# Kernel tuning notes

Measured on AMD Instinct MI355X. Metric: run time of the kernel, lower is better.

The kernel has to match this reference:

```python
import jax, jax.numpy as jnp
import numpy as np

B, D_OUT, SEQ = 4, 512, 4000
N_LABELS, E_DIM = 8929, 300


def setup_inputs() -> dict:
    key = jax.random.key(0)
    k1, k2, k3, k4 = jax.random.split(key, 4)
    H = jax.random.normal(k1, (B, D_OUT, SEQ), dtype=jnp.float32)
    label_emb = jax.random.normal(k2, (N_LABELS, E_DIM), dtype=jnp.float32)  # Q.weight
    W_map = jax.random.normal(k3, (D_OUT, E_DIM), dtype=jnp.float32) * 0.05  # conv1d k=1 weight [out,in]
    b_map = jax.random.normal(k4, (D_OUT,), dtype=jnp.float32) * 0.05
    return {"H": H, "label_emb": label_emb, "W_map": W_map, "b_map": b_map}


def reference(H, label_emb, W_map, b_map):
    # mapping_layer(Q.weight.T).T : kernel-size-1 conv == linear over embedding dim
    Q = jnp.einsum('oe,le->lo', W_map, label_emb) + b_map  # [n_labels, d_out]
    # E = Q @ H ; H is [b, d_out, seq] -> E [b, n_labels, seq] (scale=False)
    E = jnp.einsum('ld,bds->bls', Q, H)
    A = jax.nn.softmax(E, axis=2)                          # softmax over sequence
    C = jnp.einsum('bls,bds->bld', A, H)                   # A @ H^T -> [b, n_labels, d_out]
    return C, A
```

## Files before the change

kernel.cpp:

```cpp
#include <hip/hip_runtime.h>

#define BB 4
#define DD 512
#define SS 4000
#define LL 8929
#define EE 300

typedef __attribute__((ext_vector_type(8))) short bhalf8;
typedef __attribute__((ext_vector_type(4))) float floatx4;
typedef __attribute__((ext_vector_type(4))) unsigned short us4;

struct HS { unsigned short h, l; };

__device__ __forceinline__ HS splitR(float x) {
  unsigned u = __builtin_bit_cast(unsigned, x);
  unsigned hb = (u + 0x7FFFu + ((u >> 16) & 1u)) >> 16;
  float hf = __builtin_bit_cast(float, hb << 16);
  float r = x - hf;
  unsigned v = __builtin_bit_cast(unsigned, r);
  unsigned lb = (v + 0x7FFFu + ((v >> 16) & 1u)) >> 16;
  HS o; o.h = (unsigned short)hb; o.l = (unsigned short)lb;
  return o;
}

__device__ __forceinline__ HS splitT(float x) {
  unsigned u = __builtin_bit_cast(unsigned, x);
  float hf = __builtin_bit_cast(float, u & 0xFFFF0000u);
  float r = x - hf;
  HS o;
  o.h = (unsigned short)(u >> 16);
  o.l = (unsigned short)(__builtin_bit_cast(unsigned, r) >> 16);
  return o;
}

__device__ __forceinline__ void gld16(const unsigned short* g, void* l) {
  __builtin_amdgcn_global_load_lds(
      (const __attribute__((address_space(1))) unsigned int*)g,
      (__attribute__((address_space(3))) unsigned int*)l, 16, 0, 0);
}

__global__ __launch_bounds__(256) void gemm_e(
    const unsigned short* __restrict__ Qh, const unsigned short* __restrict__ Ql,
    const unsigned short* __restrict__ Hth, const unsigned short* __restrict__ Htl,
    float* __restrict__ Eg) {
  __shared__ __align__(16) unsigned short Ah_s[128 * 32];
  __shared__ __align__(16) unsigned short Al_s[128 * 32];
  __shared__ __align__(16) unsigned short Bh_s[128 * 32];
  __shared__ __align__(16) unsigned short Bl_s[128 * 32];

  const unsigned short* Bhp = Hth + (long)blockIdx.z * SS * DD;
  const unsigned short* Blp = Htl + (long)blockIdx.z * SS * DD;
  float* E = Eg + (long)blockIdx.z * LL * SS;

  const int t = threadIdx.x, lane = t & 63, w = t >> 6;
  const int m0 = blockIdx.y * 128, n0 = blockIdx.x * 128;
  const int wm = (w >> 1) * 64, wn = (w & 1) * 64;
  const int lr = lane & 15;

  const int srow = lane >> 2;
  const int sch = ((lane & 3) ^ ((lane >> 3) & 3)) * 8;
  const int r0 = w * 32 + srow, r1 = r0 + 16;
  const long am0 = (long)((m0 + r0 < LL) ? m0 + r0 : LL - 1) * DD;
  const long am1 = (long)((m0 + r1 < LL) ? m0 + r1 : LL - 1) * DD;
  const long bn0 = (long)((n0 + r0 < SS) ? n0 + r0 : SS - 1) * DD;
  const long bn1 = (long)((n0 + r1 < SS) ? n0 + r1 : SS - 1) * DD;
  char* const dA = (char*)Ah_s + w * 2048;
  char* const dAl = (char*)Al_s + w * 2048;
  char* const dB = (char*)Bh_s + w * 2048;
  char* const dBl = (char*)Bl_s + w * 2048;

  const int chA = (((lane >> 4) ^ ((lr >> 1) & 3))) * 16;
  const int raB = (wm + lr) * 64 + chA;
  const int rbB = (wn + lr) * 64 + chA;

  floatx4 acc[4][4];
#pragma unroll
  for (int i = 0; i < 4; ++i)
#pragma unroll
    for (int j = 0; j < 4; ++j) acc[i][j] = (floatx4){0.f, 0.f, 0.f, 0.f};

  for (int kb = 0; kb < DD; kb += 32) {
    __syncthreads();
    gld16(Qh + am0 + kb + sch, dA);
    gld16(Qh + am1 + kb + sch, dA + 1024);
    gld16(Ql + am0 + kb + sch, dAl);
    gld16(Ql + am1 + kb + sch, dAl + 1024);
    gld16(Bhp + bn0 + kb + sch, dB);
    gld16(Bhp + bn1 + kb + sch, dB + 1024);
    gld16(Blp + bn0 + kb + sch, dBl);
    gld16(Blp + bn1 + kb + sch, dBl + 1024);
    __syncthreads();

    bhalf8 ah[4], al[4], bh[4], bl[4];
#pragma unroll
    for (int f = 0; f < 4; ++f) {
      ah[f] = *(const bhalf8*)((const char*)Ah_s + raB + f * 1024);
      al[f] = *(const bhalf8*)((const char*)Al_s + raB + f * 1024);
      bh[f] = *(const bhalf8*)((const char*)Bh_s + rbB + f * 1024);
      bl[f] = *(const bhalf8*)((const char*)Bl_s + rbB + f * 1024);
    }
#pragma unroll
    for (int i = 0; i < 4; ++i)
#pragma unroll
      for (int j = 0; j < 4; ++j) {
        acc[i][j] = __builtin_amdgcn_mfma_f32_16x16x32_bf16(ah[i], bh[j], acc[i][j], 0, 0, 0);
        acc[i][j] = __builtin_amdgcn_mfma_f32_16x16x32_bf16(ah[i], bl[j], acc[i][j], 0, 0, 0);
        acc[i][j] = __builtin_amdgcn_mfma_f32_16x16x32_bf16(al[i], bh[j], acc[i][j], 0, 0, 0);
      }
  }

  const int cr = (lane >> 4) * 4;
#pragma unroll
  for (int i = 0; i < 4; ++i)
#pragma unroll
    for (int j = 0; j < 4; ++j)
#pragma unroll
      for (int r = 0; r < 4; ++r) {
        const int m = m0 + wm + i * 16 + cr + r;
        const int n = n0 + wn + j * 16 + lr;
        if (m < LL && n < SS) E[(long)m * SS + n] = acc[i][j][r];
      }
}

__global__ __launch_bounds__(256) void gemm_c(
    const float* __restrict__ Ag, const unsigned short* __restrict__ Hh,
    const unsigned short* __restrict__ Hl, float* __restrict__ Cg) {
  __shared__ __align__(16) unsigned short Ah_s[128][40];
  __shared__ __align__(16) unsigned short Al_s[128][40];
  __shared__ __align__(16) unsigned short Bh_s[128 * 32];
  __shared__ __align__(16) unsigned short Bl_s[128 * 32];

  const float* A = Ag + (long)blockIdx.z * LL * SS;
  const unsigned short* Bhp = Hh + (long)blockIdx.z * DD * SS;
  const unsigned short* Blp = Hl + (long)blockIdx.z * DD * SS;
  float* C = Cg + (long)blockIdx.z * LL * DD;

  const int t = threadIdx.x, lane = t & 63, w = t >> 6;
  const int m0 = blockIdx.y * 128, n0 = blockIdx.x * 128;
  const int wm = (w >> 1) * 64, wn = (w & 1) * 64;
  const int lr = lane & 15;

  const int srow = lane >> 2;
  const int sch = ((lane & 3) ^ ((lane >> 3) & 3)) * 8;
  const long bn0 = (long)(n0 + w * 32 + srow) * SS;
  const long bn1 = bn0 + (long)16 * SS;
  char* const dB = (char*)Bh_s + w * 2048;
  char* const dBl = (char*)Bl_s + w * 2048;

  const int sr = t >> 3;
  const int scol = (t & 7) * 4;

  const int chB = (((lane >> 4) ^ ((lr >> 1) & 3))) * 16;
  const int rbB = (wn + lr) * 64 + chB;
  const int raBytes = (lane >> 4) * 16;

  floatx4 acc[4][4];
#pragma unroll
  for (int i = 0; i < 4; ++i)
#pragma unroll
    for (int j = 0; j < 4; ++j) acc[i][j] = (floatx4){0.f, 0.f, 0.f, 0.f};

  for (int kb = 0; kb < SS; kb += 32) {
    __syncthreads();
    gld16(Bhp + bn0 + kb + sch, dB);
    gld16(Bhp + bn1 + kb + sch, dB + 1024);
    gld16(Blp + bn0 + kb + sch, dBl);
    gld16(Blp + bn1 + kb + sch, dBl + 1024);
#pragma unroll
    for (int rr = 0; rr < 4; ++rr) {
      const int row = rr * 32 + sr;
      const int m = m0 + row;
      float4 v = make_float4(0.f, 0.f, 0.f, 0.f);
      if (m < LL) v = *reinterpret_cast<const float4*>(A + (long)m * SS + kb + scol);
      HS p0 = splitT(v.x), p1 = splitT(v.y), p2 = splitT(v.z), p3 = splitT(v.w);
      us4 h, l;
      h.x = p0.h; l.x = p0.l; h.y = p1.h; l.y = p1.l;
      h.z = p2.h; l.z = p2.l; h.w = p3.h; l.w = p3.l;
      *reinterpret_cast<us4*>(&Ah_s[row][scol]) = h;
      *reinterpret_cast<us4*>(&Al_s[row][scol]) = l;
    }
    __syncthreads();

    bhalf8 ah[4], al[4], bh[4], bl[4];
#pragma unroll
    for (int f = 0; f < 4; ++f) {
      ah[f] = *(const bhalf8*)((const char*)&Ah_s[wm + f * 16 + lr][0] + raBytes);
      al[f] = *(const bhalf8*)((const char*)&Al_s[wm + f * 16 + lr][0] + raBytes);
      bh[f] = *(const bhalf8*)((const char*)Bh_s + rbB + f * 1024);
      bl[f] = *(const bhalf8*)((const char*)Bl_s + rbB + f * 1024);
    }
#pragma unroll
    for (int i = 0; i < 4; ++i)
#pragma unroll
      for (int j = 0; j < 4; ++j) {
        acc[i][j] = __builtin_amdgcn_mfma_f32_16x16x32_bf16(ah[i], bh[j], acc[i][j], 0, 0, 0);
        acc[i][j] = __builtin_amdgcn_mfma_f32_16x16x32_bf16(ah[i], bl[j], acc[i][j], 0, 0, 0);
        acc[i][j] = __builtin_amdgcn_mfma_f32_16x16x32_bf16(al[i], bh[j], acc[i][j], 0, 0, 0);
      }
  }

  const int cr = (lane >> 4) * 4;
#pragma unroll
  for (int i = 0; i < 4; ++i)
#pragma unroll
    for (int j = 0; j < 4; ++j)
#pragma unroll
      for (int r = 0; r < 4; ++r) {
        const int m = m0 + wm + i * 16 + cr + r;
        const int n = n0 + wn + j * 16 + lr;
        if (m < LL) C[(long)m * DD + n] = acc[i][j][r];
      }
}

__global__ __launch_bounds__(256) void split_transpose(
    const float* __restrict__ H, unsigned short* __restrict__ Th,
    unsigned short* __restrict__ Tl) {
  __shared__ float tile[32][33];
  const int b = blockIdx.z;
  const int s0 = blockIdx.x * 32, d0 = blockIdx.y * 32;
  const int tx = threadIdx.x & 31, ty = threadIdx.x >> 5;
  const float* Hb = H + (long)b * DD * SS;
#pragma unroll
  for (int i = 0; i < 4; ++i)
    tile[ty + i * 8][tx] = Hb[(long)(d0 + ty + i * 8) * SS + s0 + tx];
  __syncthreads();
  unsigned short* Thb = Th + (long)b * SS * DD;
  unsigned short* Tlb = Tl + (long)b * SS * DD;
#pragma unroll
  for (int i = 0; i < 4; ++i) {
    HS p = splitR(tile[tx][ty + i * 8]);
    const long o = (long)(s0 + ty + i * 8) * DD + d0 + tx;
    Thb[o] = p.h;
    Tlb[o] = p.l;
  }
}

__global__ __launch_bounds__(256) void back_transpose(
    const unsigned short* __restrict__ Th, const unsigned short* __restrict__ Tl,
    unsigned short* __restrict__ Hh, unsigned short* __restrict__ Hl) {
  __shared__ unsigned short th[32][33], tl[32][33];
  const int b = blockIdx.z;
  const int s0 = blockIdx.x * 32, d0 = blockIdx.y * 32;
  const int tx = threadIdx.x & 31, ty = threadIdx.x >> 5;
  const unsigned short* Tb = Th + (long)b * SS * DD;
  const unsigned short* Tlb = Tl + (long)b * SS * DD;
#pragma unroll
  for (int i = 0; i < 4; ++i) {
    const long o = (long)(s0 + ty + i * 8) * DD + d0 + tx;
    th[ty + i * 8][tx] = Tb[o];
    tl[ty + i * 8][tx] = Tlb[o];
  }
  __syncthreads();
  unsigned short* Hhb = Hh + (long)b * DD * SS;
  unsigned short* Hlb = Hl + (long)b * DD * SS;
#pragma unroll
  for (int i = 0; i < 4; ++i) {
    const long o = (long)(d0 + ty + i * 8) * SS + s0 + tx;
    Hhb[o] = th[tx][ty + i * 8];
    Hlb[o] = tl[tx][ty + i * 8];
  }
}

__global__ __launch_bounds__(256) void gemm_q(
    const float* __restrict__ Ag, const float* __restrict__ Bg,
    const float* __restrict__ bias, unsigned short* __restrict__ Qh,
    unsigned short* __restrict__ Ql, int M, int N, int K) {
  __shared__ float As[16][132];
  __shared__ float Bs[16][132];
  const int t = threadIdx.x;
  const int m0 = blockIdx.y * 128, n0 = blockIdx.x * 128;
  const int tx = t & 15, ty = t >> 4;
  float acc[8][8];
#pragma unroll
  for (int i = 0; i < 8; ++i)
#pragma unroll
    for (int j = 0; j < 8; ++j) acc[i][j] = 0.f;
  const int ra = t >> 2;
  const int kc = (t & 3) * 4;
  const int KT = (K + 15) / 16;
  for (int kt = 0; kt < KT; ++kt) {
    const int kb = kt * 16;
#pragma unroll
    for (int h = 0; h < 2; ++h) {
      const int mrow = ra + h * 64;
      const int m = m0 + mrow, k = kb + kc;
      float4 v = make_float4(0.f, 0.f, 0.f, 0.f);
      if (m < M && k < K)
        v = *reinterpret_cast<const float4*>(Ag + (long)m * K + k);
      As[kc + 0][mrow] = v.x; As[kc + 1][mrow] = v.y;
      As[kc + 2][mrow] = v.z; As[kc + 3][mrow] = v.w;
      const int n = n0 + mrow;
      float4 u = make_float4(0.f, 0.f, 0.f, 0.f);
      if (n < N && k < K)
        u = *reinterpret_cast<const float4*>(Bg + (long)n * K + k);
      Bs[kc + 0][mrow] = u.x; Bs[kc + 1][mrow] = u.y;
      Bs[kc + 2][mrow] = u.z; Bs[kc + 3][mrow] = u.w;
    }
    __syncthreads();
#pragma unroll
    for (int kk = 0; kk < 16; ++kk) {
      const float4 a0 = *reinterpret_cast<const float4*>(&As[kk][ty * 8]);
      const float4 a1 = *reinterpret_cast<const float4*>(&As[kk][ty * 8 + 4]);
      const float4 b0 = *reinterpret_cast<const float4*>(&Bs[kk][tx * 8]);
      const float4 b1 = *reinterpret_cast<const float4*>(&Bs[kk][tx * 8 + 4]);
      const float a[8] = {a0.x, a0.y, a0.z, a0.w, a1.x, a1.y, a1.z, a1.w};
      const float b[8] = {b0.x, b0.y, b0.z, b0.w, b1.x, b1.y, b1.z, b1.w};
#pragma unroll
      for (int i = 0; i < 8; ++i)
#pragma unroll
        for (int j = 0; j < 8; ++j) acc[i][j] = fmaf(a[i], b[j], acc[i][j]);
    }
    __syncthreads();
  }
#pragma unroll
  for (int i = 0; i < 8; ++i) {
    const int m = m0 + ty * 8 + i;
    if (m >= M) continue;
#pragma unroll
    for (int j = 0; j < 8; ++j) {
      const int n = n0 + tx * 8 + j;
      if (n < N) {
        HS p = splitR(acc[i][j] + bias[n]);
        Qh[(long)m * N + n] = p.h;
        Ql[(long)m * N + n] = p.l;
      }
    }
  }
}

__global__ __launch_bounds__(256) void softmax4000(float* __restrict__ P) {
  float* p = P + (long)blockIdx.x * SS;
  const int t = threadIdx.x;
  float v[16];
  float mx = -1e30f;
#pragma unroll
  for (int j = 0; j < 16; ++j) {
    const int i = t + j * 256;
    if (i < SS) { v[j] = p[i]; mx = fmaxf(mx, v[j]); } else v[j] = -1e30f;
  }
#pragma unroll
  for (int o = 32; o > 0; o >>= 1) mx = fmaxf(mx, __shfl_xor(mx, o));
  __shared__ float rm[4], rs[4];
  const int w = t >> 6;
  if ((t & 63) == 0) rm[w] = mx;
  __syncthreads();
  mx = fmaxf(fmaxf(rm[0], rm[1]), fmaxf(rm[2], rm[3]));
  float s = 0.f;
#pragma unroll
  for (int j = 0; j < 16; ++j) {
    const int i = t + j * 256;
    if (i < SS) { v[j] = __expf(v[j] - mx); s += v[j]; }
  }
#pragma unroll
  for (int o = 32; o > 0; o >>= 1) s += __shfl_xor(s, o);
  if ((t & 63) == 0) rs[w] = s;
  __syncthreads();
  s = rs[0] + rs[1] + rs[2] + rs[3];
  const float inv = 1.f / s;
#pragma unroll
  for (int j = 0; j < 16; ++j) {
    const int i = t + j * 256;
    if (i < SS) p[i] = v[j] * inv;
  }
}

extern "C" void kernel_launch(void* const* d_in, const int* in_sizes, int n_in,
                              void* d_out, int out_size, void* d_ws,
                              size_t ws_size, hipStream_t stream) {
  const float* H = (const float*)d_in[0];
  const float* lab = (const float*)d_in[1];
  const float* Wm = (const float*)d_in[2];
  const float* bm = (const float*)d_in[3];

  float* Cout = (float*)d_out;
  float* Aout = Cout + (size_t)BB * LL * DD;
  unsigned short* Qh = (unsigned short*)Cout;
  unsigned short* Ql = Qh + (size_t)LL * DD;

  unsigned short* Hth = (unsigned short*)d_ws;
  unsigned short* Htl = Hth + (size_t)BB * SS * DD;

  unsigned short* Hh = (unsigned short*)d_in[0];
  unsigned short* Hl = Hh + (size_t)BB * DD * SS;

  const dim3 blk(256);
  const int MB = (LL + 127) / 128;

  split_transpose<<<dim3(SS / 32, DD / 32, BB), blk, 0, stream>>>(H, Hth, Htl);

  back_transpose<<<dim3(SS / 32, DD / 32, BB), blk, 0, stream>>>(Hth, Htl, Hh, Hl);

  gemm_q<<<dim3(DD / 128, MB, 1), blk, 0, stream>>>(lab, Wm, bm, Qh, Ql, LL, DD, EE);

  gemm_e<<<dim3((SS + 127) / 128, MB, BB), blk, 0, stream>>>(Qh, Ql, Hth, Htl, Aout);

  softmax4000<<<dim3(BB * LL), blk, 0, stream>>>(Aout);

  gemm_c<<<dim3(DD / 128, MB, BB), blk, 0, stream>>>(Aout, Hh, Hl, Cout);
}
```

Before: 2.112 ms.

## Double-buffer LDS tiles in gemm_e and gemm_c to overlap loads with MFMA

```diff
diff --git a/kernel.cpp b/kernel.cpp
--- a/kernel.cpp
+++ b/kernel.cpp
@@ -6,6 +6,7 @@
 #define LL 8929
 #define EE 300
 
+typedef unsigned short ushortt;
 typedef __attribute__((ext_vector_type(8))) short bhalf8;
 typedef __attribute__((ext_vector_type(4))) float floatx4;
 typedef __attribute__((ext_vector_type(4))) unsigned short us4;
@@ -40,16 +41,16 @@
 }
 
 __global__ __launch_bounds__(256) void gemm_e(
-    const unsigned short* __restrict__ Qh, const unsigned short* __restrict__ Ql,
-    const unsigned short* __restrict__ Hth, const unsigned short* __restrict__ Htl,
+    const ushortt* __restrict__ Qh, const ushortt* __restrict__ Ql,
+    const ushortt* __restrict__ Hth, const ushortt* __restrict__ Htl,
     float* __restrict__ Eg) {
-  __shared__ __align__(16) unsigned short Ah_s[128 * 32];
-  __shared__ __align__(16) unsigned short Al_s[128 * 32];
-  __shared__ __align__(16) unsigned short Bh_s[128 * 32];
-  __shared__ __align__(16) unsigned short Bl_s[128 * 32];
-
-  const unsigned short* Bhp = Hth + (long)blockIdx.z * SS * DD;
-  const unsigned short* Blp = Htl + (long)blockIdx.z * SS * DD;
+  __shared__ __align__(16) ushortt Ah_s[2][4096];
+  __shared__ __align__(16) ushortt Al_s[2][4096];
+  __shared__ __align__(16) ushortt Bh_s[2][4096];
+  __shared__ __align__(16) ushortt Bl_s[2][4096];
+
+  const ushortt* Bhp = Hth + (long)blockIdx.z * SS * DD;
+  const ushortt* Blp = Htl + (long)blockIdx.z * SS * DD;
   float* E = Eg + (long)blockIdx.z * LL * SS;
 
   const int t = threadIdx.x, lane = t & 63, w = t >> 6;
@@ -64,10 +65,6 @@
   const long am1 = (long)((m0 + r1 < LL) ? m0 + r1 : LL - 1) * DD;
   const long bn0 = (long)((n0 + r0 < SS) ? n0 + r0 : SS - 1) * DD;
   const long bn1 = (long)((n0 + r1 < SS) ? n0 + r1 : SS - 1) * DD;
-  char* const dA = (char*)Ah_s + w * 2048;
-  char* const dAl = (char*)Al_s + w * 2048;
-  char* const dB = (char*)Bh_s + w * 2048;
-  char* const dBl = (char*)Bl_s + w * 2048;
 
   const int chA = (((lane >> 4) ^ ((lr >> 1) & 3))) * 16;
   const int raB = (wm + lr) * 64 + chA;
@@ -79,25 +76,47 @@
 #pragma unroll
     for (int j = 0; j < 4; ++j) acc[i][j] = (floatx4){0.f, 0.f, 0.f, 0.f};
 
-  for (int kb = 0; kb < DD; kb += 32) {
-    __syncthreads();
-    gld16(Qh + am0 + kb + sch, dA);
-    gld16(Qh + am1 + kb + sch, dA + 1024);
-    gld16(Ql + am0 + kb + sch, dAl);
-    gld16(Ql + am1 + kb + sch, dAl + 1024);
-    gld16(Bhp + bn0 + kb + sch, dB);
-    gld16(Bhp + bn1 + kb + sch, dB + 1024);
-    gld16(Blp + bn0 + kb + sch, dBl);
-    gld16(Blp + bn1 + kb + sch, dBl + 1024);
-    __syncthreads();
-
+  {
+    char* dA = (char*)Ah_s[0] + w * 2048;
+    char* dAl = (char*)Al_s[0] + w * 2048;
+    char* dB = (char*)Bh_s[0] + w * 2048;
+    char* dBl = (char*)Bl_s[0] + w * 2048;
+    gld16(Qh + am0 + sch, dA);
+    gld16(Qh + am1 + sch, dA + 1024);
+    gld16(Ql + am0 + sch, dAl);
+    gld16(Ql + am1 + sch, dAl + 1024);
+    gld16(Bhp + bn0 + sch, dB);
+    gld16(Bhp + bn1 + sch, dB + 1024);
+    gld16(Blp + bn0 + sch, dBl);
+    gld16(Blp + bn1 + sch, dBl + 1024);
+  }
+  __syncthreads();
+
+  const int KT = DD / 32;
+  for (int kt = 0; kt < KT; ++kt) {
+    const int cb = kt & 1, nb = cb ^ 1;
+    if (kt + 1 < KT) {
+      const int kb = (kt + 1) * 32;
+      char* dA = (char*)Ah_s[nb] + w * 2048;
+      char* dAl = (char*)Al_s[nb] + w * 2048;
+      char* dB = (char*)Bh_s[nb] + w * 2048;
+      char* dBl = (char*)Bl_s[nb] + w * 2048;
+      gld16(Qh + am0 + kb + sch, dA);
+      gld16(Qh + am1 + kb + sch, dA + 1024);
+      gld16(Ql + am0 + kb + sch, dAl);
+      gld16(Ql + am1 + kb + sch, dAl + 1024);
+      gld16(Bhp + bn0 + kb + sch, dB);
+      gld16(Bhp + bn1 + kb + sch, dB + 1024);
+      gld16(Blp + bn0 + kb + sch, dBl);
+      gld16(Blp + bn1 + kb + sch, dBl + 1024);
+    }
     bhalf8 ah[4], al[4], bh[4], bl[4];
 #pragma unroll
     for (int f = 0; f < 4; ++f) {
-      ah[f] = *(const bhalf8*)((const char*)Ah_s + raB + f * 1024);
-      al[f] = *(const bhalf8*)((const char*)Al_s + raB + f * 1024);
-      bh[f] = *(const bhalf8*)((const char*)Bh_s + rbB + f * 1024);
-      bl[f] = *(const bhalf8*)((const char*)Bl_s + rbB + f * 1024);
+      ah[f] = *(const bhalf8*)((const char*)Ah_s[cb] + raB + f * 1024);
+      al[f] = *(const bhalf8*)((const char*)Al_s[cb] + raB + f * 1024);
+      bh[f] = *(const bhalf8*)((const char*)Bh_s[cb] + rbB + f * 1024);
+      bl[f] = *(const bhalf8*)((const char*)Bl_s[cb] + rbB + f * 1024);
     }
 #pragma unroll
     for (int i = 0; i < 4; ++i)
@@ -107,6 +126,7 @@
         acc[i][j] = __builtin_amdgcn_mfma_f32_16x16x32_bf16(ah[i], bl[j], acc[i][j], 0, 0, 0);
         acc[i][j] = __builtin_amdgcn_mfma_f32_16x16x32_bf16(al[i], bh[j], acc[i][j], 0, 0, 0);
       }
+    __syncthreads();
   }
 
   const int cr = (lane >> 4) * 4;
@@ -123,16 +143,16 @@
 }
 
 __global__ __launch_bounds__(256) void gemm_c(
-    const float* __restrict__ Ag, const unsigned short* __restrict__ Hh,
-    const unsigned short* __restrict__ Hl, float* __restrict__ Cg) {
-  __shared__ __align__(16) unsigned short Ah_s[128][40];
-  __shared__ __align__(16) unsigned short Al_s[128][40];
-  __shared__ __align__(16) unsigned short Bh_s[128 * 32];
-  __shared__ __align__(16) unsigned short Bl_s[128 * 32];
+    const float* __restrict__ Ag, const ushortt* __restrict__ Hh,
+    const ushortt* __restrict__ Hl, float* __restrict__ Cg) {
+  __shared__ __align__(16) ushortt Bh_s[2][4096];
+  __shared__ __align__(16) ushortt Bl_s[2][4096];
+  __shared__ __align__(16) ushortt Ah_s[2][128][40];
+  __shared__ __align__(16) ushortt Al_s[2][128][40];
 
   const float* A = Ag + (long)blockIdx.z * LL * SS;
-  const unsigned short* Bhp = Hh + (long)blockIdx.z * DD * SS;
-  const unsigned short* Blp = Hl + (long)blockIdx.z * DD * SS;
+  const ushortt* Bhp = Hh + (long)blockIdx.z * DD * SS;
+  const ushortt* Blp = Hl + (long)blockIdx.z * DD * SS;
   float* C = Cg + (long)blockIdx.z * LL * DD;
 
   const int t = threadIdx.x, lane = t & 63, w = t >> 6;
@@ -144,8 +164,6 @@
   const int sch = ((lane & 3) ^ ((lane >> 3) & 3)) * 8;
   const long bn0 = (long)(n0 + w * 32 + srow) * SS;
   const long bn1 = bn0 + (long)16 * SS;
-  char* const dB = (char*)Bh_s + w * 2048;
-  char* const dBl = (char*)Bl_s + w * 2048;
 
   const int sr = t >> 3;
   const int scol = (t & 7) * 4;
@@ -160,34 +178,60 @@
 #pragma unroll
     for (int j = 0; j < 4; ++j) acc[i][j] = (floatx4){0.f, 0.f, 0.f, 0.f};
 
-  for (int kb = 0; kb < SS; kb += 32) {
-    __syncthreads();
-    gld16(Bhp + bn0 + kb + sch, dB);
-    gld16(Bhp + bn1 + kb + sch, dB + 1024);
-    gld16(Blp + bn0 + kb + sch, dBl);
-    gld16(Blp + bn1 + kb + sch, dBl + 1024);
+  float4 av[4];
+  {
+    char* dB = (char*)Bh_s[0] + w * 2048;
+    char* dBl = (char*)Bl_s[0] + w * 2048;
+    gld16(Bhp + bn0 + sch, dB);
+    gld16(Bhp + bn1 + sch, dB + 1024);
+    gld16(Blp + bn0 + sch, dBl);
+    gld16(Blp + bn1 + sch, dBl + 1024);
+#pragma unroll
+    for (int rr = 0; rr < 4; ++rr) {
+      const int m = m0 + rr * 32 + sr;
+      av[rr] = make_float4(0.f, 0.f, 0.f, 0.f);
+      if (m < LL) av[rr] = *reinterpret_cast<const float4*>(A + (long)m * SS + scol);
+    }
 #pragma unroll
     for (int rr = 0; rr < 4; ++rr) {
       const int row = rr * 32 + sr;
-      const int m = m0 + row;
-      float4 v = make_float4(0.f, 0.f, 0.f, 0.f);
-      if (m < LL) v = *reinterpret_cast<const float4*>(A + (long)m * SS + kb + scol);
-      HS p0 = splitT(v.x), p1 = splitT(v.y), p2 = splitT(v.z), p3 = splitT(v.w);
+      HS p0 = splitT(av[rr].x), p1 = splitT(av[rr].y);
+      HS p2 = splitT(av[rr].z), p3 = splitT(av[rr].w);
       us4 h, l;
       h.x = p0.h; l.x = p0.l; h.y = p1.h; l.y = p1.l;
       h.z = p2.h; l.z = p2.l; h.w = p3.h; l.w = p3.l;
-      *reinterpret_cast<us4*>(&Ah_s[row][scol]) = h;
-      *reinterpret_cast<us4*>(&Al_s[row][scol]) = l;
-    }
-    __syncthreads();
-
+      *reinterpret_cast<us4*>(&Ah_s[0][row][scol]) = h;
+      *reinterpret_cast<us4*>(&Al_s[0][row][scol]) = l;
+    }
+  }
+  __syncthreads();
+
+  const int KT = SS / 32;
+  for (int kt = 0; kt < KT; ++kt) {
+    const int cb = kt & 1, nb = cb ^ 1;
+    const bool pf = (kt + 1 < KT);
+    if (pf) {
+      const int kb = (kt + 1) * 32;
+      char* dB = (char*)Bh_s[nb] + w * 2048;
+      char* dBl = (char*)Bl_s[nb] + w * 2048;
+      gld16(Bhp + bn0 + kb + sch, dB);
+      gld16(Bhp + bn1 + kb + sch, dB + 1024);
+      gld16(Blp + bn0 + kb + sch, dBl);
+      gld16(Blp + bn1 + kb + sch, dBl + 1024);
+#pragma unroll
+      for (int rr = 0; rr < 4; ++rr) {
+        const int m = m0 + rr * 32 + sr;
+        av[rr] = make_float4(0.f, 0.f, 0.f, 0.f);
+        if (m < LL) av[rr] = *reinterpret_cast<const float4*>(A + (long)m * SS + kb + scol);
+      }
+    }
     bhalf8 ah[4], al[4], bh[4], bl[4];
 #pragma unroll
     for (int f = 0; f < 4; ++f) {
-      ah[f] = *(const bhalf8*)((const char*)&Ah_s[wm + f * 16 + lr][0] + raBytes);
-      al[f] = *(const bhalf8*)((const char*)&Al_s[wm + f * 16 + lr][0] + raBytes);
-      bh[f] = *(const bhalf8*)((const char*)Bh_s + rbB + f * 1024);
-      bl[f] = *(const bhalf8*)((const char*)Bl_s + rbB + f * 1024);
+      ah[f] = *(const bhalf8*)((const char*)&Ah_s[cb][wm + f * 16 + lr][0] + raBytes);
+      al[f] = *(const bhalf8*)((const char*)&Al_s[cb][wm + f * 16 + lr][0] + raBytes);
+      bh[f] = *(const bhalf8*)((const char*)Bh_s[cb] + rbB + f * 1024);
+      bl[f] = *(const bhalf8*)((const char*)Bl_s[cb] + rbB + f * 1024);
     }
 #pragma unroll
     for (int i = 0; i < 4; ++i)
@@ -197,6 +241,20 @@
         acc[i][j] = __builtin_amdgcn_mfma_f32_16x16x32_bf16(ah[i], bl[j], acc[i][j], 0, 0, 0);
         acc[i][j] = __builtin_amdgcn_mfma_f32_16x16x32_bf16(al[i], bh[j], acc[i][j], 0, 0, 0);
       }
+    if (pf) {
+#pragma unroll
+      for (int rr = 0; rr < 4; ++rr) {
+        const int row = rr * 32 + sr;
+        HS p0 = splitT(av[rr].x), p1 = splitT(av[rr].y);
+        HS p2 = splitT(av[rr].z), p3 = splitT(av[rr].w);
+        us4 h, l;
+        h.x = p0.h; l.x = p0.l; h.y = p1.h; l.y = p1.l;
+        h.z = p2.h; l.z = p2.l; h.w = p3.h; l.w = p3.l;
+        *reinterpret_cast<us4*>(&Ah_s[nb][row][scol]) = h;
+        *reinterpret_cast<us4*>(&Al_s[nb][row][scol]) = l;
+      }
+    }
+    __syncthreads();
   }
 
   const int cr = (lane >> 4) * 4;
@@ -213,8 +271,8 @@
 }
 
 __global__ __launch_bounds__(256) void split_transpose(
-    const float* __restrict__ H, unsigned short* __restrict__ Th,
-    unsigned short* __restrict__ Tl) {
+    const float* __restrict__ H, ushortt* __restrict__ Th,
+    ushortt* __restrict__ Tl) {
   __shared__ float tile[32][33];
   const int b = blockIdx.z;
   const int s0 = blockIdx.x * 32, d0 = blockIdx.y * 32;
@@ -224,8 +282,8 @@
   for (int i = 0; i < 4; ++i)
     tile[ty + i * 8][tx] = Hb[(long)(d0 + ty + i * 8) * SS + s0 + tx];
   __syncthreads();
-  unsigned short* Thb = Th + (long)b * SS * DD;
-  unsigned short* Tlb = Tl + (long)b * SS * DD;
+  ushortt* Thb = Th + (long)b * SS * DD;
+  ushortt* Tlb = Tl + (long)b * SS * DD;
 #pragma unroll
   for (int i = 0; i < 4; ++i) {
     HS p = splitR(tile[tx][ty + i * 8]);
@@ -236,14 +294,14 @@
 }
 
 __global__ __launch_bounds__(256) void back_transpose(
-    const unsigned short* __restrict__ Th, const unsigned short* __restrict__ Tl,
-    unsigned short* __restrict__ Hh, unsigned short* __restrict__ Hl) {
-  __shared__ unsigned short th[32][33], tl[32][33];
+    const ushortt* __restrict__ Th, const ushortt* __restrict__ Tl,
+    ushortt* __restrict__ Hh, ushortt* __restrict__ Hl) {
+  __shared__ ushortt th[32][33], tl[32][33];
   const int b = blockIdx.z;
   const int s0 = blockIdx.x * 32, d0 = blockIdx.y * 32;
   const int tx = threadIdx.x & 31, ty = threadIdx.x >> 5;
-  const unsigned short* Tb = Th + (long)b * SS * DD;
-  const unsigned short* Tlb = Tl + (long)b * SS * DD;
+  const ushortt* Tb = Th + (long)b * SS * DD;
+  const ushortt* Tlb = Tl + (long)b * SS * DD;
 #pragma unroll
   for (int i = 0; i < 4; ++i) {
     const long o = (long)(s0 + ty + i * 8) * DD + d0 + tx;
@@ -251,8 +309,8 @@
     tl[ty + i * 8][tx] = Tlb[o];
   }
   __syncthreads();
-  unsigned short* Hhb = Hh + (long)b * DD * SS;
-  unsigned short* Hlb = Hl + (long)b * DD * SS;
+  ushortt* Hhb = Hh + (long)b * DD * SS;
+  ushortt* Hlb = Hl + (long)b * DD * SS;
 #pragma unroll
   for (int i = 0; i < 4; ++i) {
     const long o = (long)(d0 + ty + i * 8) * SS + s0 + tx;
@@ -263,8 +321,8 @@
 
 __global__ __launch_bounds__(256) void gemm_q(
     const float* __restrict__ Ag, const float* __restrict__ Bg,
-    const float* __restrict__ bias, unsigned short* __restrict__ Qh,
-    unsigned short* __restrict__ Ql, int M, int N, int K) {
+    const float* __restrict__ bias, ushortt* __restrict__ Qh,
+    ushortt* __restrict__ Ql, int M, int N, int K) {
   __shared__ float As[16][132];
   __shared__ float Bs[16][132];
   const int t = threadIdx.x;
@@ -374,14 +432,14 @@
 
   float* Cout = (float*)d_out;
   float* Aout = Cout + (size_t)BB * LL * DD;
-  unsigned short* Qh = (unsigned short*)Cout;
-  unsigned short* Ql = Qh + (size_t)LL * DD;
-
-  unsigned short* Hth = (unsigned short*)d_ws;
-  unsigned short* Htl = Hth + (size_t)BB * SS * DD;
-
-  unsigned short* Hh = (unsigned short*)d_in[0];
-  unsigned short* Hl = Hh + (size_t)BB * DD * SS;
+  ushortt* Qh = (ushortt*)Cout;
+  ushortt* Ql = Qh + (size_t)LL * DD;
+
+  ushortt* Hth = (ushortt*)d_ws;
+  ushortt* Htl = Hth + (size_t)BB * SS * DD;
+
+  ushortt* Hh = (ushortt*)d_in[0];
+  ushortt* Hl = Hh + (size_t)BB * DD * SS;
 
   const dim3 blk(256);
   const int MB = (LL + 127) / 128;
```

New measurement: 2.034 ms. 3.7% less time.
